# Kernel optimization log

Hardware: AMD Instinct MI355X
Metric: run time of the kernel (lower is better)

Reference implementation:

```python
import jax, jax.numpy as jnp
import numpy as np

TEMPERATURE = 0.01
VMIN, VMAX = -1.0, 1.0
NUM_VALUES = 256


def setup_inputs() -> dict:
    key = jax.random.key(0)
    k_img, k_cmap = jax.random.split(key)
    image = jax.random.uniform(k_img, (4, 3, 512, 512), dtype=jnp.float32)
    cmap = jax.random.uniform(k_cmap, (NUM_VALUES, 3), dtype=jnp.float32)
    idx = jnp.arange(NUM_VALUES, dtype=jnp.float32)
    v_i = VMIN + (VMAX - VMIN) * idx / (NUM_VALUES - 1)
    return {"image": image, "cmap": cmap, "v_i": v_i}


def reference(image, cmap, v_i):
    # image: (N, 3, H, W) -> (N, H, W, 3)
    img = jnp.transpose(image, (0, 2, 3, 1))
    # squared euclidean distance to each of the 256 colormap colors
    # dist[n,h,w,k] = sum_c (img[n,h,w,c] - cmap[k,c])^2
    diff = img[..., None, :] - cmap  # (N, H, W, K, 3)
    distances = jnp.sum(diff * diff, axis=-1)  # (N, H, W, K)
    weights = jax.nn.softmax(-distances / TEMPERATURE, axis=-1)
    velocities = jnp.einsum('nhwk,k->nhw', weights, v_i)
    return velocities
```

## Files before the change

kernel.cpp:

```cpp
#include <hip/hip_runtime.h>


typedef float v2f __attribute__((ext_vector_type(2)));

#define HWSZ 262144
#define NPIX 1048576
#define K2F  144.2695040888963f

__global__ __launch_bounds__(256) void rgb2vel_prep(
    const float* __restrict__ cmap, const float* __restrict__ v_i,
    float4* __restrict__ ab, float* __restrict__ vv) {
  int k = threadIdx.x;
  float cx = cmap[k * 3 + 0];
  float cy = cmap[k * 3 + 1];
  float cz = cmap[k * 3 + 2];
  float4 r;
  r.x = 2.0f * K2F * cx;
  r.y = 2.0f * K2F * cy;
  r.z = 2.0f * K2F * cz;
  r.w = -K2F * (cx * cx + cy * cy + cz * cz);
  ab[k] = r;
  vv[k] = v_i[k];
}

__global__ __launch_bounds__(256) void rgb2vel_main(
    const float* __restrict__ img, const float4* __restrict__ ab,
    const float* __restrict__ vv, float* __restrict__ out) {
  int t = blockIdx.x * 256 + threadIdx.x;
  int n = t >> 17;
  int hw2 = (t & 131071) << 1;
  const float* base = img + (size_t)n * 3 * HWSZ + hw2;
  v2f px = {base[0], base[1]};
  v2f py = {base[HWSZ], base[HWSZ + 1]};
  v2f pz = {base[2 * HWSZ], base[2 * HWSZ + 1]};

  v2f mk2 = {-K2F, -K2F};
  v2f cp = __builtin_elementwise_fma(
               px, px, __builtin_elementwise_fma(py, py, pz * pz)) *
           mk2;

  v2f s = {0.0f, 0.0f};
  v2f sv = {0.0f, 0.0f};
#pragma unroll 16
  for (int k = 0; k < 256; ++k) {
    float4 c = ab[k];
    v2f cx = {c.x, c.x};
    v2f cy = {c.y, c.y};
    v2f cz = {c.z, c.z};
    v2f cw = {c.w, c.w};
    v2f a = __builtin_elementwise_fma(
        cx, px,
        __builtin_elementwise_fma(cy, py,
                                  __builtin_elementwise_fma(cz, pz, cw + cp)));
    v2f w;
    w.x = __builtin_amdgcn_exp2f(a.x);
    w.y = __builtin_amdgcn_exp2f(a.y);
    s = s + w;
    float vk = vv[k];
    v2f vkv = {vk, vk};
    sv = __builtin_elementwise_fma(w, vkv, sv);
  }
  float o0 = sv.x / s.x;
  float o1 = sv.y / s.y;
  size_t o = (size_t)2 * t;
  out[o] = o0;
  out[o + 1] = o1;
}

extern "C" void kernel_launch(void* const* d_in, const int* in_sizes, int n_in,
                              void* d_out, int out_size, void* d_ws, size_t ws_size,
                              hipStream_t stream) {
  const float* image = (const float*)d_in[0];
  const float* cmap  = (const float*)d_in[1];
  const float* v_i   = (const float*)d_in[2];
  float* out = (float*)d_out;

  float4* ab = (float4*)d_ws;
  float*  vv = (float*)((char*)d_ws + 256 * 16);

  rgb2vel_prep<<<1, 256, 0, stream>>>(cmap, v_i, ab, vv);
  rgb2vel_main<<<NPIX / 2 / 256, 256, 0, stream>>>(image, ab, vv, out);
}
```

Before: 103.7 us.

## Replace hardware exp2 with cubic polynomial plus ldexp and process four pixels per thread

Each thread now handles four pixels instead of two, halving the grid and amortizing the per-k colormap loads across more work. The transcendental v_exp_f32 is replaced by round-to-nearest, a cubic polynomial on the fraction and v_ldexp_f32, moving work from the transcendental unit onto packed FMA pipes. The cost is more VALU instructions per element, reduced accuracy of exp2 (a cubic approximation), and higher register pressure with fewer waves in flight.

```diff
diff --git a/kernel.cpp b/kernel.cpp
--- a/kernel.cpp
+++ b/kernel.cpp
@@ -6,6 +6,12 @@
 #define HWSZ 262144
 #define NPIX 1048576
 #define K2F  144.2695040888963f
+
+__device__ __forceinline__ float ldexp_hw(float x, int n) {
+  float r;
+  asm("v_ldexp_f32 %0, %1, %2" : "=v"(r) : "v"(x), "v"(n));
+  return r;
+}
 
 __global__ __launch_bounds__(256) void rgb2vel_prep(
     const float* __restrict__ cmap, const float* __restrict__ v_i,
@@ -27,20 +33,31 @@
     const float* __restrict__ img, const float4* __restrict__ ab,
     const float* __restrict__ vv, float* __restrict__ out) {
   int t = blockIdx.x * 256 + threadIdx.x;
-  int n = t >> 17;
-  int hw2 = (t & 131071) << 1;
-  const float* base = img + (size_t)n * 3 * HWSZ + hw2;
-  v2f px = {base[0], base[1]};
-  v2f py = {base[HWSZ], base[HWSZ + 1]};
-  v2f pz = {base[2 * HWSZ], base[2 * HWSZ + 1]};
+  int n = t >> 16;
+  int hw4 = (t & 65535) << 2;
+  const float* base = img + (size_t)n * 3 * HWSZ + hw4;
+  v2f px0 = {base[0], base[1]};
+  v2f px1 = {base[2], base[3]};
+  v2f py0 = {base[HWSZ], base[HWSZ + 1]};
+  v2f py1 = {base[HWSZ + 2], base[HWSZ + 3]};
+  v2f pz0 = {base[2 * HWSZ], base[2 * HWSZ + 1]};
+  v2f pz1 = {base[2 * HWSZ + 2], base[2 * HWSZ + 3]};
 
   v2f mk2 = {-K2F, -K2F};
-  v2f cp = __builtin_elementwise_fma(
-               px, px, __builtin_elementwise_fma(py, py, pz * pz)) *
-           mk2;
+  v2f cp0 = __builtin_elementwise_fma(
+                px0, px0, __builtin_elementwise_fma(py0, py0, pz0 * pz0)) *
+            mk2;
+  v2f cp1 = __builtin_elementwise_fma(
+                px1, px1, __builtin_elementwise_fma(py1, py1, pz1 * pz1)) *
+            mk2;
 
-  v2f s = {0.0f, 0.0f};
-  v2f sv = {0.0f, 0.0f};
+  const v2f C3 = {0.0555041f, 0.0555041f};
+  const v2f C2 = {0.2426310f, 0.2426310f};
+  const v2f C1 = {0.6931472f, 0.6931472f};
+  const v2f C0 = {0.9999249f, 0.9999249f};
+
+  v2f s0 = {0.0f, 0.0f}, s1 = {0.0f, 0.0f};
+  v2f sv0 = {0.0f, 0.0f}, sv1 = {0.0f, 0.0f};
 #pragma unroll 16
   for (int k = 0; k < 256; ++k) {
     float4 c = ab[k];
@@ -48,23 +65,46 @@
     v2f cy = {c.y, c.y};
     v2f cz = {c.z, c.z};
     v2f cw = {c.w, c.w};
-    v2f a = __builtin_elementwise_fma(
-        cx, px,
-        __builtin_elementwise_fma(cy, py,
-                                  __builtin_elementwise_fma(cz, pz, cw + cp)));
-    v2f w;
-    w.x = __builtin_amdgcn_exp2f(a.x);
-    w.y = __builtin_amdgcn_exp2f(a.y);
-    s = s + w;
+    v2f a0 = __builtin_elementwise_fma(
+        cx, px0,
+        __builtin_elementwise_fma(
+            cy, py0, __builtin_elementwise_fma(cz, pz0, cw + cp0)));
+    v2f a1 = __builtin_elementwise_fma(
+        cx, px1,
+        __builtin_elementwise_fma(
+            cy, py1, __builtin_elementwise_fma(cz, pz1, cw + cp1)));
+    v2f nf0, nf1;
+    nf0.x = __builtin_rintf(a0.x);
+    nf0.y = __builtin_rintf(a0.y);
+    nf1.x = __builtin_rintf(a1.x);
+    nf1.y = __builtin_rintf(a1.y);
+    v2f r0 = a0 - nf0;
+    v2f r1 = a1 - nf1;
+    v2f p0 = __builtin_elementwise_fma(
+        __builtin_elementwise_fma(__builtin_elementwise_fma(C3, r0, C2), r0,
+                                  C1),
+        r0, C0);
+    v2f p1 = __builtin_elementwise_fma(
+        __builtin_elementwise_fma(__builtin_elementwise_fma(C3, r1, C2), r1,
+                                  C1),
+        r1, C0);
+    v2f w0, w1;
+    w0.x = ldexp_hw(p0.x, (int)nf0.x);
+    w0.y = ldexp_hw(p0.y, (int)nf0.y);
+    w1.x = ldexp_hw(p1.x, (int)nf1.x);
+    w1.y = ldexp_hw(p1.y, (int)nf1.y);
+    s0 = s0 + w0;
+    s1 = s1 + w1;
     float vk = vv[k];
     v2f vkv = {vk, vk};
-    sv = __builtin_elementwise_fma(w, vkv, sv);
+    sv0 = __builtin_elementwise_fma(w0, vkv, sv0);
+    sv1 = __builtin_elementwise_fma(w1, vkv, sv1);
   }
-  float o0 = sv.x / s.x;
-  float o1 = sv.y / s.y;
-  size_t o = (size_t)2 * t;
-  out[o] = o0;
-  out[o + 1] = o1;
+  size_t o = (size_t)4 * t;
+  out[o + 0] = sv0.x / s0.x;
+  out[o + 1] = sv0.y / s0.y;
+  out[o + 2] = sv1.x / s1.x;
+  out[o + 3] = sv1.y / s1.y;
 }
 
 extern "C" void kernel_launch(void* const* d_in, const int* in_sizes, int n_in,
@@ -79,5 +119,5 @@
   float*  vv = (float*)((char*)d_ws + 256 * 16);
 
   rgb2vel_prep<<<1, 256, 0, stream>>>(cmap, v_i, ab, vv);
-  rgb2vel_main<<<NPIX / 2 / 256, 256, 0, stream>>>(image, ab, vv, out);
+  rgb2vel_main<<<NPIX / 4 / 256, 256, 0, stream>>>(image, ab, vv, out);
 }
```

Measured after the change: 126.8 us. 22.3% more time.
